# Kernel optimization log

Hardware: AMD Instinct MI355X
Metric: run time of the kernel (lower is better)

Reference implementation:

```python
import math
import jax, jax.numpy as jnp
import numpy as np

D = 1024      # d_model
FF = 4096     # d_ff
E = 8         # num_experts
K = 2         # num_selected (top-k)
R = 2         # lora_rank (hardcoded in ToyMoEClassifier)
ALPHA = 4.0   # lora_alpha (hardcoded)
SCALE = ALPHA / R
CF = 1.25     # capacity_factor
NCLS = 2      # head output classes


def setup_inputs() -> dict:
    key = jax.random.key(0)
    ks = jax.random.split(key, 11)
    B, S = 4, 2048
    x = jax.random.normal(ks[0], (B, S, D), jnp.float32)
    Wg = jax.random.normal(ks[1], (D, E), jnp.float32) * 0.02
    W1 = jax.random.normal(ks[2], (D, FF), jnp.float32) * 0.02
    W2 = jax.random.normal(ks[3], (FF, D), jnp.float32) * 0.02
    A1 = jax.random.normal(ks[4], (E, D, R), jnp.float32) * 0.02
    B1 = jax.random.normal(ks[5], (E, R, FF), jnp.float32) * 0.02
    A2 = jax.random.normal(ks[6], (E, FF, R), jnp.float32) * 0.02
    B2 = jax.random.normal(ks[7], (E, R, D), jnp.float32) * 0.02
    Wh = jax.random.normal(ks[8], (D, NCLS), jnp.float32) * 0.02
    bh = jnp.zeros((NCLS,), jnp.float32)
    return {"x": x, "Wg": Wg, "W1": W1, "W2": W2, "A1": A1, "B1": B1,
            "A2": A2, "B2": B2, "Wh": Wh, "bh": bh}


def _moe_lora(x, Wg, W1, W2, A1, B1, A2, B2):
    B, S, d = x.shape
    T = B * S
    tok = x.reshape(T, d)                                  # [T, d]
    logits = tok @ Wg                                      # [T, E]
    vals, idx = jax.lax.top_k(logits, K)                   # [T, K]
    gates = jax.nn.softmax(vals, axis=-1)                  # renormalize over selected

    C = int(math.ceil(CF * T * K / E))                     # expert capacity (static)

    # position within expert, slot-major priority (slot 0 tokens first)
    onehot = jax.nn.one_hot(idx, E, dtype=jnp.float32)     # [T, K, E]
    m = onehot.transpose(1, 0, 2).reshape(K * T, E)        # [K*T, E]
    pos = jnp.cumsum(m, axis=0) - m
    pos_in = jnp.sum(pos * m, axis=-1).astype(jnp.int32)   # [K*T]
    exp_flat = idx.T.reshape(K * T)                        # [K*T]
    keep = (pos_in < C)
    w = gates.T.reshape(K * T) * keep.astype(gates.dtype)  # combine weight
    slot_idx = exp_flat * C + jnp.minimum(pos_in, C - 1)   # flat [E*C] index

    # dispatch: scatter kept tokens into per-expert capacity buffers
    disp = jnp.zeros((E * C, d), tok.dtype)
    for s in range(K):  # K is tiny and static
        sl = slice(s * T, (s + 1) * T)
        disp = disp.at[slot_idx[sl]].add(tok * keep[sl][:, None].astype(tok.dtype))
    disp3 = disp.reshape(E, C, d)

    # per-expert LoRA FFN: base weights shared, low-rank adapters per expert
    h = jax.nn.gelu(jnp.einsum('ecd,df->ecf', disp3, W1)
                    + SCALE * jnp.einsum('ecr,erf->ecf',
                                         jnp.einsum('ecd,edr->ecr', disp3, A1), B1))
    y = (jnp.einsum('ecf,fd->ecd', h, W2)
         + SCALE * jnp.einsum('ecr,erd->ecd',
                              jnp.einsum('ecf,efr->ecr', h, A2), B2))
    y_flat = y.reshape(E * C, d)

    # combine: gather expert outputs back, weighted by gates (dropped tokens -> 0)
    out = jnp.zeros((T, d), x.dtype)
    for s in range(K):
        sl = slice(s * T, (s + 1) * T)
        out = out + y_flat[slot_idx[sl]] * w[sl][:, None]
    return out.reshape(B, S, d)


def reference(x, Wg, W1, W2, A1, B1, A2, B2, Wh, bh):
    out = _moe_lora(x, Wg, W1, W2, A1, B1, A2, B2)   # [B, S, D]
    pooled = out.mean(axis=1)                        # [B, D]
    return pooled @ Wh + bh                          # [B, NCLS]
```

## Files before the change

### kernel.cpp

```cpp
#include <hip/hip_runtime.h>
#include <hip/hip_bf16.h>
#include <cstdint>
#include <cstddef>

#define D_MODEL 1024
#define FF_DIM  4096
#define NEXP    8
#define TOK     8192
#define CAP     2560
#define ECAP    (NEXP*CAP)
#define LSCALE  2.0f
#define SA_BYTE 124
#define SB_BYTE 122

typedef __attribute__((ext_vector_type(8))) int   int32x8;
typedef __attribute__((ext_vector_type(4))) float f32x4;
typedef __attribute__((ext_vector_type(2))) float f32x2;

__device__ __forceinline__ void gload16(const void* g, void* l){
  __builtin_amdgcn_global_load_lds((const __attribute__((address_space(1))) void*)g,
                                   (__attribute__((address_space(3))) void*)l, 16, 0, 0);
}
__device__ __forceinline__ float gelu_tanh(float x){
  float u = 0.7978845608028654f * (x + 0.044715f * x * x * x);
  float e = __expf(2.0f * u);
  float t = 1.0f - 2.0f / (e + 1.0f);
  return 0.5f * x * (1.0f + t);
}

__global__ void prep_kernel(const float* __restrict__ x, const float* __restrict__ Wg,
                            int* __restrict__ exp_flat, float* __restrict__ g_flat,
                            float* __restrict__ pooled, float* __restrict__ wslot,
                            const float* __restrict__ W1, const float* __restrict__ W2,
                            uint8_t* __restrict__ W1q, uint8_t* __restrict__ W2q)
{
  __shared__ float tile[64][65];
  int bx = blockIdx.x;
  int tid = threadIdx.x;
  if (bx < 2048){
    int gid = bx * 256 + tid;
    if (gid < 4*D_MODEL) pooled[gid] = 0.f;
    else if (gid < 4*D_MODEL + ECAP) wslot[gid - 4*D_MODEL] = 0.f;
    int lane = tid & 63;
    int wave = tid >> 6;
    int t = bx * 4 + wave;
    const float4* xv = (const float4*)(x + (size_t)t * D_MODEL);
    float acc[8];
#pragma unroll
    for (int e = 0; e < 8; e++) acc[e] = 0.f;
#pragma unroll
    for (int i = 0; i < 4; i++){
      int i4 = lane + i*64;
      float4 v = xv[i4];
#pragma unroll
      for (int k = 0; k < 4; k++){
        float xs = (&v.x)[k];
        const float4* wr = (const float4*)(Wg + (size_t)(i4*4 + k) * 8);
        float4 w0 = wr[0], w1 = wr[1];
        acc[0] += xs*w0.x; acc[1] += xs*w0.y; acc[2] += xs*w0.z; acc[3] += xs*w0.w;
        acc[4] += xs*w1.x; acc[5] += xs*w1.y; acc[6] += xs*w1.z; acc[7] += xs*w1.w;
      }
    }
#pragma unroll
    for (int off = 32; off > 0; off >>= 1){
#pragma unroll
      for (int e = 0; e < 8; e++) acc[e] += __shfl_down(acc[e], off);
    }
    if (lane == 0){
      float m0 = acc[0]; int e0 = 0;
#pragma unroll
      for (int e = 1; e < 8; e++) if (acc[e] > m0){ m0 = acc[e]; e0 = e; }
      float m1 = -3.4e38f; int e1 = 0;
#pragma unroll
      for (int e = 0; e < 8; e++) if (e != e0 && acc[e] > m1){ m1 = acc[e]; e1 = e; }
      float z = __expf(m1 - m0);
      float inv = 1.f / (1.f + z);
      exp_flat[t]       = e0;
      exp_flat[TOK + t] = e1;
      g_flat[t]         = inv;
      g_flat[TOK + t]   = z * inv;
    }
  } else {
    int b = bx - 2048;
    int z = b >> 10; b &= 1023;
    int bxx = b & 15, byy = b >> 4;
    const float* src; uint8_t* dst; int srcld, dstld, a0, b0;
    if (z == 0){ src = W1; dst = W1q; srcld = FF_DIM; dstld = D_MODEL; a0 = bxx*64; b0 = byy*64; }
    else       { src = W2; dst = W2q; srcld = D_MODEL; dstld = FF_DIM; a0 = byy*64; b0 = bxx*64; }
    int r  = tid >> 4;
    int c4 = (tid & 15) * 4;
#pragma unroll
    for (int i = 0; i < 4; i++){
      int al = r + i*16;
      float4 v = *(const float4*)(src + (size_t)(a0 + al) * srcld + b0 + c4);
      tile[al][c4+0] = v.x; tile[al][c4+1] = v.y; tile[al][c4+2] = v.z; tile[al][c4+3] = v.w;
    }
    __syncthreads();
#pragma unroll
    for (int i = 0; i < 4; i++){
      int bl = r + i*16;
      int bb = b0 + bl;
      int pk = __builtin_amdgcn_cvt_pk_fp8_f32(32.f*tile[c4+0][bl], 32.f*tile[c4+1][bl], 0, false);
      pk     = __builtin_amdgcn_cvt_pk_fp8_f32(32.f*tile[c4+2][bl], 32.f*tile[c4+3][bl], pk, true);
      *(int*)(dst + (size_t)bb * dstld + a0 + c4) = pk;
    }
  }
}

__global__ __launch_bounds__(1024) void route_all(const int* __restrict__ exp_flat,
                                                  const float* __restrict__ g_flat,
                                                  int* __restrict__ slotidx,
                                                  float* __restrict__ wcomb,
                                                  int* __restrict__ fillc)
{
  __shared__ uint8_t rnk[16384];
  __shared__ uint8_t eexp[16384];
  __shared__ int     cnt[256*8];
  __shared__ int     grpoff[64];
  int tid = threadIdx.x;
  int lane = tid & 63, wv = tid >> 6;
  unsigned long long ltmask = (1ull << lane) - 1ull;
  for (int c = wv; c < 256; c += 16){
    int j = c*64 + lane;
    int e = exp_flat[j];
    eexp[j] = (uint8_t)e;
    int r = 0, myc = 0;
#pragma unroll
    for (int q = 0; q < 8; q++){
      unsigned long long m = __ballot(e == q);
      if (e == q) r = __popcll(m & ltmask);
      if (lane == q) myc = __popcll(m);
    }
    rnk[j] = (uint8_t)r;
    if (lane < 8) cnt[c*8 + lane] = myc;
  }
  __syncthreads();
  if (wv == 0){
    int e = lane & 7, g = lane >> 3;
    int run = 0;
    for (int c = g*32; c < g*32 + 32; c++){
      int v = cnt[c*8 + e];
      cnt[c*8 + e] = run;
      run += v;
    }
    int offs = 0, tot = 0;
#pragma unroll
    for (int gg = 0; gg < 8; gg++){
      int v = __shfl(run, gg*8 + e);
      if (gg < g) offs += v;
      tot += v;
    }
    grpoff[lane] = offs;
    if (g == 0) fillc[e] = tot < CAP ? tot : CAP;
  }
  __syncthreads();
  for (int j = tid; j < 16384; j += 1024){
    int e = eexp[j];
    int c = j >> 6;
    int pos = cnt[c*8 + e] + grpoff[(c >> 5)*8 + e] + rnk[j];
    bool keep = pos < CAP;
    slotidx[j] = e*CAP + (keep ? pos : (CAP-1));
    wcomb[j]   = keep ? g_flat[j] : 0.f;
  }
}

__global__ void dispatch_kernel(const float* __restrict__ x, const int* __restrict__ slotidx,
                                const float* __restrict__ wcomb, uint8_t* __restrict__ dispA,
                                float* __restrict__ wslot, int* __restrict__ tbat,
                                const float* __restrict__ A1, float* __restrict__ U1)
{
  int j = blockIdx.x;
  float w = wcomb[j];
  if (w == 0.f) return;
  int t = j & (TOK - 1);
  int slot = slotidx[j];
  int e = slot / CAP;
  int i = threadIdx.x;
  const float4* src = (const float4*)(x + (size_t)t * D_MODEL);
  float4 a = src[2*i], b = src[2*i+1];
  int p0 = __builtin_amdgcn_cvt_pk_fp8_f32(8.f*a.x, 8.f*a.y, 0, false);
  p0     = __builtin_amdgcn_cvt_pk_fp8_f32(8.f*a.z, 8.f*a.w, p0, true);
  int p1 = __builtin_amdgcn_cvt_pk_fp8_f32(8.f*b.x, 8.f*b.y, 0, false);
  p1     = __builtin_amdgcn_cvt_pk_fp8_f32(8.f*b.z, 8.f*b.w, p1, true);
  int2 o; o.x = p0; o.y = p1;
  *(int2*)(dispA + (size_t)slot * D_MODEL + i*8) = o;
  const float2* Av = (const float2*)(A1 + (size_t)e * D_MODEL * 2);
  int d0 = i*8;
  float xs[8] = {a.x,a.y,a.z,a.w,b.x,b.y,b.z,b.w};
  float pa = 0.f, pb = 0.f;
#pragma unroll
  for (int k = 0; k < 8; k++){
    float2 w2 = Av[d0 + k];
    pa += xs[k]*w2.x; pb += xs[k]*w2.y;
  }
#pragma unroll
  for (int off = 32; off > 0; off >>= 1){
    pa += __shfl_down(pa, off);
    pb += __shfl_down(pb, off);
  }
  __shared__ float red[4];
  int lane = i & 63, wv = i >> 6;
  if (lane == 0){ red[wv*2] = pa; red[wv*2+1] = pb; }
  __syncthreads();
  if (i == 0){
    U1[slot*2+0] = red[0] + red[2];
    U1[slot*2+1] = red[1] + red[3];
    wslot[slot] = w; tbat[slot] = t >> 11;
  }
}

__global__ void lora_u(const uint8_t* __restrict__ X, const float* __restrict__ Aw,
                       float* __restrict__ U, int Kdim)
{
  int lane = threadIdx.x & 63;
  int wv   = threadIdx.x >> 6;
  int slot = blockIdx.x * 4 + wv;
  int e = slot / CAP;
  const int4*   row = (const int4*)(X + (size_t)slot * Kdim);
  const float2* Av  = (const float2*)(Aw + (size_t)e * Kdim * 2);
  float a0 = 0.f, a1 = 0.f;
  int n16 = Kdim >> 4;
  for (int i = lane; i < n16; i += 64){
    int4 v = row[i];
    int d = i * 16;
#pragma unroll
    for (int c = 0; c < 4; c++){
      int w = (&v.x)[c];
      f32x2 f01 = __builtin_amdgcn_cvt_pk_f32_fp8(w, false);
      f32x2 f23 = __builtin_amdgcn_cvt_pk_f32_fp8(w, true);
      int dd = d + c*4;
      float2 w0 = Av[dd], w1 = Av[dd+1], w2 = Av[dd+2], w3 = Av[dd+3];
      a0 += f01.x*w0.x + f01.y*w1.x + f23.x*w2.x + f23.y*w3.x;
      a1 += f01.x*w0.y + f01.y*w1.y + f23.x*w2.y + f23.y*w3.y;
    }
  }
#pragma unroll
  for (int off = 32; off > 0; off >>= 1){
    a0 += __shfl_down(a0, off);
    a1 += __shfl_down(a1, off);
  }
  if (lane == 0){ U[slot*2] = a0 * 0.125f; U[slot*2+1] = a1 * 0.125f; }
}

template<bool GELU, bool COMBINE>
__global__ __launch_bounds__(256, 4) void gemm_mx(const uint8_t* __restrict__ A,
                                                  const uint8_t* __restrict__ Bt,
                                                  uint8_t* __restrict__ Cb,
                                                  int K, int N, const int* __restrict__ fillc,
                                                  const float* __restrict__ U,
                                                  const float* __restrict__ Bl,
                                                  const float* __restrict__ wslot,
                                                  const int* __restrict__ tbat,
                                                  float* __restrict__ pooled)
{
  int e = blockIdx.x / 40;
  if ((blockIdx.x % 40) * 64 >= fillc[e]) return;
  int row0 = blockIdx.x * 64;
  int col0 = blockIdx.y * 128;

  __shared__ __align__(16) uint8_t As[64*128];
  __shared__ __align__(16) uint8_t Bs[128*128];
  __shared__ float part[COMBINE ? 512 : 4];

  int tid  = threadIdx.x;
  int lane = tid & 63;
  int wave = tid >> 6;
  int wm = wave & 1, wn = wave >> 1;

  if (COMBINE){ part[tid] = 0.f; part[tid + 256] = 0.f; }

  int r8 = lane >> 3;
  int cs = (lane & 7) ^ r8;
  const uint8_t* gA = A  + (size_t)(row0 + wave*16 + r8) * K + cs*16;
  const uint8_t* gB = Bt + (size_t)(col0 + wave*32 + r8) * K + cs*16;
  uint8_t* lA = As + wave*16*128;
  uint8_t* lB = Bs + wave*32*128;

  int rb = lane & 15;
  int q  = lane >> 4;

  f32x4 acc[2][4];
#pragma unroll
  for (int i = 0; i < 2; i++)
#pragma unroll
    for (int j = 0; j < 4; j++)
      acc[i][j] = (f32x4){0.f, 0.f, 0.f, 0.f};

  for (int k0 = 0; k0 < K; k0 += 128){
    __syncthreads();
#pragma unroll
    for (int g = 0; g < 2; g++)
      gload16(gA + k0 + (size_t)g*8*K, lA + g*1024);
#pragma unroll
    for (int g = 0; g < 4; g++)
      gload16(gB + k0 + (size_t)g*8*K, lB + g*1024);
    __syncthreads();
    int32x8 a[2], b[4];
#pragma unroll
    for (int mt = 0; mt < 2; mt++){
      int row = wm*32 + mt*16 + rb;
      const uint8_t* base = As + row*128;
      int sw = row & 7;
      int4 lo = *(const int4*)(base + (((2*q)  ^sw)*16));
      int4 hi = *(const int4*)(base + (((2*q+1)^sw)*16));
      int32x8 v; v[0]=lo.x; v[1]=lo.y; v[2]=lo.z; v[3]=lo.w;
                 v[4]=hi.x; v[5]=hi.y; v[6]=hi.z; v[7]=hi.w;
      a[mt] = v;
    }
#pragma unroll
    for (int nt = 0; nt < 4; nt++){
      int row = wn*64 + nt*16 + rb;
      const uint8_t* base = Bs + row*128;
      int sw = row & 7;
      int4 lo = *(const int4*)(base + (((2*q)  ^sw)*16));
      int4 hi = *(const int4*)(base + (((2*q+1)^sw)*16));
      int32x8 v; v[0]=lo.x; v[1]=lo.y; v[2]=lo.z; v[3]=lo.w;
                 v[4]=hi.x; v[5]=hi.y; v[6]=hi.z; v[7]=hi.w;
      b[nt] = v;
    }
#pragma unroll
    for (int mt = 0; mt < 2; mt++)
#pragma unroll
      for (int nt = 0; nt < 4; nt++)
        acc[mt][nt] = __builtin_amdgcn_mfma_scale_f32_16x16x128_f8f6f4(
            a[mt], b[nt], acc[mt][nt], 0, 0, 0, SA_BYTE, 0, SB_BYTE);
  }

  float b0c[4], b1c[4];
#pragma unroll
  for (int nt = 0; nt < 4; nt++){
    int col = col0 + wn*64 + rb + nt*16;
    b0c[nt] = Bl[(e*2+0)*N + col];
    b1c[nt] = Bl[(e*2+1)*N + col];
  }

#pragma unroll
  for (int mt = 0; mt < 2; mt++){
#pragma unroll
    for (int r = 0; r < 4; r++){
      int row = row0 + wm*32 + mt*16 + q*4 + r;
      float2 u = *(const float2*)(U + row*2);
      float wv = 0.f; int tb = 0;
      if (COMBINE){ wv = wslot[row]; tb = tbat[row]; }
      size_t base = (size_t)row * N + col0 + wn*64 + rb;
#pragma unroll
      for (int nt = 0; nt < 4; nt++){
        float v = acc[mt][nt][r] + LSCALE*(u.x*b0c[nt] + u.y*b1c[nt]);
        if (GELU){
          v = gelu_tanh(v);
          int pk = __builtin_amdgcn_cvt_pk_fp8_f32(8.f*v, 0.f, 0, false);
          Cb[base + nt*16] = (uint8_t)(pk & 0xFF);
        }
        if (COMBINE){
          if (wv != 0.f) atomicAdd(&part[tb*128 + wn*64 + rb + nt*16], wv*v);
        }
      }
    }
  }

  if (COMBINE){
    __syncthreads();
#pragma unroll
    for (int idx = tid; idx < 512; idx += 256){
      float pv = part[idx];
      if (pv != 0.f) atomicAdd(pooled + (size_t)(idx >> 7) * D_MODEL + col0 + (idx & 127), pv);
    }
  }
}

__global__ void head_kernel(const float* __restrict__ pooled, const float* __restrict__ Wh,
                            const float* __restrict__ bh, float* __restrict__ out)
{
  int lane = threadIdx.x & 63;
  int wave = threadIdx.x >> 6;
  int b = wave >> 1, c = wave & 1;
  float s = 0.f;
#pragma unroll
  for (int i = 0; i < 16; i++){
    int d = lane + i*64;
    s += pooled[(size_t)b * D_MODEL + d] * Wh[d*2 + c];
  }
#pragma unroll
  for (int off = 32; off > 0; off >>= 1) s += __shfl_down(s, off);
  if (lane == 0) out[b*2 + c] = s * (1.0f/2048.0f) + bh[c];
}

extern "C" void kernel_launch(void* const* d_in, const int* in_sizes, int n_in,
                              void* d_out, int out_size, void* d_ws, size_t ws_size,
                              hipStream_t stream)
{
  const float* x  = (const float*)d_in[0];
  const float* Wg = (const float*)d_in[1];
  const float* W1 = (const float*)d_in[2];
  const float* W2 = (const float*)d_in[3];
  const float* A1 = (const float*)d_in[4];
  const float* B1 = (const float*)d_in[5];
  const float* A2 = (const float*)d_in[6];
  const float* B2 = (const float*)d_in[7];
  const float* Wh = (const float*)d_in[8];
  const float* bh = (const float*)d_in[9];
  float* out = (float*)d_out;

  char* p = (char*)d_ws;
  auto alloc = [&](size_t bytes){
    char* r = p;
    p += (bytes + 255) & ~(size_t)255;
    return (void*)r;
  };
  uint8_t* W1q   = (uint8_t*)alloc((size_t)FF_DIM*D_MODEL);
  uint8_t* W2q   = (uint8_t*)alloc((size_t)D_MODEL*FF_DIM);
  uint8_t* dispA = (uint8_t*)alloc((size_t)ECAP*D_MODEL);
  uint8_t* H     = (uint8_t*)alloc((size_t)ECAP*FF_DIM);
  float* U1       = (float*)alloc((size_t)ECAP*2*4);
  float* U2       = (float*)alloc((size_t)ECAP*2*4);
  float* wslot    = (float*)alloc((size_t)ECAP*4);
  int*   tbat     = (int*)  alloc((size_t)ECAP*4);
  int*   exp_flat = (int*)  alloc((size_t)2*TOK*4);
  float* g_flat   = (float*)alloc((size_t)2*TOK*4);
  int*   slotidx  = (int*)  alloc((size_t)2*TOK*4);
  float* wcomb    = (float*)alloc((size_t)2*TOK*4);
  int*   fillc    = (int*)  alloc(256);
  float* pooled   = (float*)alloc((size_t)4*D_MODEL*4);

  prep_kernel<<<4096, 256, 0, stream>>>(x, Wg, exp_flat, g_flat, pooled, wslot,
                                        W1, W2, W1q, W2q);
  route_all<<<1, 1024, 0, stream>>>(exp_flat, g_flat, slotidx, wcomb, fillc);
  dispatch_kernel<<<2*TOK, 128, 0, stream>>>(x, slotidx, wcomb, dispA, wslot, tbat, A1, U1);
  gemm_mx<true, false><<<dim3(320,32), 256, 0, stream>>>(dispA, W1q, H, D_MODEL, FF_DIM,
                                                         fillc, U1, B1, nullptr, nullptr, nullptr);
  lora_u<<<5120, 256, 0, stream>>>(H, A2, U2, FF_DIM);
  gemm_mx<false, true><<<dim3(320,8), 256, 0, stream>>>(H, W2q, nullptr, FF_DIM, D_MODEL,
                                                        fillc, U2, B2, wslot, tbat, pooled);
  head_kernel<<<1, 512, 0, stream>>>(pooled, Wh, bh, out);
}
```

Before: 579.7 us.

## Load MFMA operands directly from global into registers with double-buffered prefetch

The GEMM kernel no longer stages A and B tiles through LDS with global_load_lds and two block barriers per K step. Each wave now loads its MFMA operand fragments straight from global memory into registers. It uses two register buffers so the next K slice is fetched while the current one is multiplied. The launch-bounds occupancy hint is dropped, and the combine scratch init moves after the main loop behind its own barrier. The cost is that waves sharing rows or columns now fetch the same data separately, so more cache traffic and register pressure may offset the removed barriers. The loop also assumes an even number of K iterations.

Result: slower. 1.127 ms (+94.5%).

```diff
diff --git a/kernel.cpp b/kernel.cpp
--- a/kernel.cpp
+++ b/kernel.cpp
@@ -17,10 +17,6 @@
 typedef __attribute__((ext_vector_type(4))) float f32x4;
 typedef __attribute__((ext_vector_type(2))) float f32x2;
 
-__device__ __forceinline__ void gload16(const void* g, void* l){
-  __builtin_amdgcn_global_load_lds((const __attribute__((address_space(1))) void*)g,
-                                   (__attribute__((address_space(3))) void*)l, 16, 0, 0);
-}
 __device__ __forceinline__ float gelu_tanh(float x){
   float u = 0.7978845608028654f * (x + 0.044715f * x * x * x);
   float e = __expf(2.0f * u);
@@ -243,23 +239,21 @@
 }
 
 template<bool GELU, bool COMBINE>
-__global__ __launch_bounds__(256, 4) void gemm_mx(const uint8_t* __restrict__ A,
-                                                  const uint8_t* __restrict__ Bt,
-                                                  uint8_t* __restrict__ Cb,
-                                                  int K, int N, const int* __restrict__ fillc,
-                                                  const float* __restrict__ U,
-                                                  const float* __restrict__ Bl,
-                                                  const float* __restrict__ wslot,
-                                                  const int* __restrict__ tbat,
-                                                  float* __restrict__ pooled)
+__global__ __launch_bounds__(256) void gemm_mx(const uint8_t* __restrict__ A,
+                                               const uint8_t* __restrict__ Bt,
+                                               uint8_t* __restrict__ Cb,
+                                               int K, int N, const int* __restrict__ fillc,
+                                               const float* __restrict__ U,
+                                               const float* __restrict__ Bl,
+                                               const float* __restrict__ wslot,
+                                               const int* __restrict__ tbat,
+                                               float* __restrict__ pooled)
 {
   int e = blockIdx.x / 40;
   if ((blockIdx.x % 40) * 64 >= fillc[e]) return;
   int row0 = blockIdx.x * 64;
   int col0 = blockIdx.y * 128;
 
-  __shared__ __align__(16) uint8_t As[64*128];
-  __shared__ __align__(16) uint8_t Bs[128*128];
   __shared__ float part[COMBINE ? 512 : 4];
 
   int tid  = threadIdx.x;
@@ -267,18 +261,12 @@
   int wave = tid >> 6;
   int wm = wave & 1, wn = wave >> 1;
 
-  if (COMBINE){ part[tid] = 0.f; part[tid + 256] = 0.f; }
-
-  int r8 = lane >> 3;
-  int cs = (lane & 7) ^ r8;
-  const uint8_t* gA = A  + (size_t)(row0 + wave*16 + r8) * K + cs*16;
-  const uint8_t* gB = Bt + (size_t)(col0 + wave*32 + r8) * K + cs*16;
-  uint8_t* lA = As + wave*16*128;
-  uint8_t* lB = Bs + wave*32*128;
-
   int rb = lane & 15;
   int q  = lane >> 4;
 
+  const uint8_t* gA = A  + (size_t)(row0 + wm*32 + rb) * K + q*32;
+  const uint8_t* gB = Bt + (size_t)(col0 + wn*64 + rb) * K + q*32;
+
   f32x4 acc[2][4];
 #pragma unroll
   for (int i = 0; i < 2; i++)
@@ -286,44 +274,43 @@
     for (int j = 0; j < 4; j++)
       acc[i][j] = (f32x4){0.f, 0.f, 0.f, 0.f};
 
-  for (int k0 = 0; k0 < K; k0 += 128){
-    __syncthreads();
-#pragma unroll
-    for (int g = 0; g < 2; g++)
-      gload16(gA + k0 + (size_t)g*8*K, lA + g*1024);
-#pragma unroll
-    for (int g = 0; g < 4; g++)
-      gload16(gB + k0 + (size_t)g*8*K, lB + g*1024);
-    __syncthreads();
-    int32x8 a[2], b[4];
+  auto loadW = [&](int k0, int32x8* a, int32x8* b){
 #pragma unroll
     for (int mt = 0; mt < 2; mt++){
-      int row = wm*32 + mt*16 + rb;
-      const uint8_t* base = As + row*128;
-      int sw = row & 7;
-      int4 lo = *(const int4*)(base + (((2*q)  ^sw)*16));
-      int4 hi = *(const int4*)(base + (((2*q+1)^sw)*16));
+      const uint8_t* p = gA + (size_t)mt*16*K + k0;
+      int4 lo = *(const int4*)p;
+      int4 hi = *(const int4*)(p + 16);
       int32x8 v; v[0]=lo.x; v[1]=lo.y; v[2]=lo.z; v[3]=lo.w;
                  v[4]=hi.x; v[5]=hi.y; v[6]=hi.z; v[7]=hi.w;
       a[mt] = v;
     }
 #pragma unroll
     for (int nt = 0; nt < 4; nt++){
-      int row = wn*64 + nt*16 + rb;
-      const uint8_t* base = Bs + row*128;
-      int sw = row & 7;
-      int4 lo = *(const int4*)(base + (((2*q)  ^sw)*16));
-      int4 hi = *(const int4*)(base + (((2*q+1)^sw)*16));
+      const uint8_t* p = gB + (size_t)nt*16*K + k0;
+      int4 lo = *(const int4*)p;
+      int4 hi = *(const int4*)(p + 16);
       int32x8 v; v[0]=lo.x; v[1]=lo.y; v[2]=lo.z; v[3]=lo.w;
                  v[4]=hi.x; v[5]=hi.y; v[6]=hi.z; v[7]=hi.w;
       b[nt] = v;
     }
+  };
+  auto compute = [&](const int32x8* a, const int32x8* b){
 #pragma unroll
     for (int mt = 0; mt < 2; mt++)
 #pragma unroll
       for (int nt = 0; nt < 4; nt++)
         acc[mt][nt] = __builtin_amdgcn_mfma_scale_f32_16x16x128_f8f6f4(
             a[mt], b[nt], acc[mt][nt], 0, 0, 0, SA_BYTE, 0, SB_BYTE);
+  };
+
+  int32x8 a0[2], b0[4], a1[2], b1[4];
+  loadW(0, a0, b0);
+  int NI = K >> 7;
+  for (int p = 0; p < NI; p += 2){
+    if (p+1 < NI) loadW((p+1) << 7, a1, b1);
+    compute(a0, b0);
+    if (p+2 < NI) loadW((p+2) << 7, a0, b0);
+    compute(a1, b1);
   }
 
   float b0c[4], b1c[4];
@@ -332,6 +319,11 @@
     int col = col0 + wn*64 + rb + nt*16;
     b0c[nt] = Bl[(e*2+0)*N + col];
     b1c[nt] = Bl[(e*2+1)*N + col];
+  }
+
+  if (COMBINE){
+    part[tid] = 0.f; part[tid + 256] = 0.f;
+    __syncthreads();
   }
 
 #pragma unroll
```
